# Performance work log

Measured on AMD Instinct MI355X. Metric: run time of the kernel, lower is better.

## Reference

```python
import jax, jax.numpy as jnp
import numpy as np

N_NODES = 50000
DROPOUT_P = 0.5


def _spmm(edge_src, edge_dst, edge_weight, h):
    # out[d] = sum_{e: dst[e]==d} w[e] * h[src[e]]  -- sparse Laplacian aggregation
    msgs = edge_weight[:, None] * h[edge_src]          # [E, F]
    return jax.ops.segment_sum(msgs, edge_dst, num_segments=N_NODES)


def setup_inputs() -> dict:
    key = jax.random.key(0)
    ks = jax.random.split(key, 8)
    E = 1600000
    nfeat, nhid, nclass = 512, 256, 40
    return {
        "x": jax.random.normal(ks[0], (N_NODES, nfeat), dtype=jnp.float32),
        "edge_src": jax.random.randint(ks[1], (E,), 0, N_NODES, dtype=jnp.int32),
        "edge_dst": jax.random.randint(ks[2], (E,), 0, N_NODES, dtype=jnp.int32),
        "edge_weight": jax.random.normal(ks[3], (E,), dtype=jnp.float32) * 0.05,
        "W1": jax.random.normal(ks[4], (nfeat, nhid), dtype=jnp.float32) * 0.05,
        "b1": jax.random.normal(ks[5], (nhid,), dtype=jnp.float32) * 0.05,
        "W2": jax.random.normal(ks[6], (nhid, nclass), dtype=jnp.float32) * 0.05,
        "b2": jax.random.normal(ks[7], (nclass,), dtype=jnp.float32) * 0.05,
    }


def reference(x, edge_src, edge_dst, edge_weight, W1, b1, W2, b2):
    # layer 1: dense GEMM -> sparse aggregate -> bias -> ReLU -> dropout
    h = x @ W1
    h = _spmm(edge_src, edge_dst, edge_weight, h)
    h = jax.nn.relu(h + b1)
    # dropout with a fixed key (deterministic, matches train-mode scaling 1/(1-p))
    keep = jax.random.bernoulli(jax.random.key(42), 1.0 - DROPOUT_P, h.shape)
    h = jnp.where(keep, h / (1.0 - DROPOUT_P), 0.0)
    # layer 2: dense GEMM -> sparse aggregate -> bias
    o = h @ W2
    o = _spmm(edge_src, edge_dst, edge_weight, o)
    return o + b2
```

## Files before the change

### kernel.cpp

```cpp
#include <hip/hip_runtime.h>

typedef short bf16x8 __attribute__((ext_vector_type(8)));
typedef float f32x4 __attribute__((ext_vector_type(4)));

constexpr int N_NODES = 50000;
constexpr int F_IN    = 512;
constexpr int F_HID   = 256;
constexpr int F_OUT   = 40;
constexpr int SCAN_BLOCKS = (N_NODES + 255) / 256;

__device__ __forceinline__ float bf2f(unsigned short u) {
  return __uint_as_float(((unsigned)u) << 16);
}
__device__ __forceinline__ unsigned short f2bf(float f) {
  unsigned x = __float_as_uint(f);
  x += 0x7FFFu + ((x >> 16) & 1u);
  return (unsigned short)(x >> 16);
}

__device__ __forceinline__ bf16x8 cvt8(f32x4 a, f32x4 b) {
  bf16x8 o;
  o[0] = (short)f2bf(a[0]); o[1] = (short)f2bf(a[1]);
  o[2] = (short)f2bf(a[2]); o[3] = (short)f2bf(a[3]);
  o[4] = (short)f2bf(b[0]); o[5] = (short)f2bf(b[1]);
  o[6] = (short)f2bf(b[2]); o[7] = (short)f2bf(b[3]);
  return o;
}

__device__ __forceinline__ unsigned tf_rotl(unsigned x, int d) {
  return (x << d) | (x >> (32 - d));
}
__device__ __forceinline__ unsigned threefry_bits(unsigned i) {
  const unsigned k0 = 0u, k1 = 42u, k2 = 0x1BD11BDAu ^ 0u ^ 42u;
  unsigned x0 = 0u + k0, x1 = i + k1;
#define TF_R(r) { x0 += x1; x1 = tf_rotl(x1, (r)) ^ x0; }
  TF_R(13) TF_R(15) TF_R(26) TF_R(6)   x0 += k1; x1 += k2 + 1u;
  TF_R(17) TF_R(29) TF_R(16) TF_R(24)  x0 += k2; x1 += k0 + 2u;
  TF_R(13) TF_R(15) TF_R(26) TF_R(6)   x0 += k0; x1 += k1 + 3u;
  TF_R(17) TF_R(29) TF_R(16) TF_R(24)  x0 += k1; x1 += k2 + 4u;
  TF_R(13) TF_R(15) TF_R(26) TF_R(6)   x0 += k2; x1 += k0 + 5u;
#undef TF_R
  return x0 ^ x1;
}

__global__ void k_zero(int* __restrict__ p, int n) {
  int i = blockIdx.x * 256 + threadIdx.x;
  if (i < n) p[i] = 0;
}

__global__ void k_hist(const int* __restrict__ dst, int* __restrict__ deg, int E) {
  int e = blockIdx.x * 256 + threadIdx.x;
  if (e < E) atomicAdd(&deg[dst[e]], 1);
}

__global__ __launch_bounds__(256) void k_scan_part(const int* __restrict__ deg,
                                                   int* __restrict__ bsum) {
  __shared__ int red[256];
  int t = threadIdx.x;
  int i = blockIdx.x * 256 + t;
  red[t] = (i < N_NODES) ? deg[i] : 0;
  __syncthreads();
#pragma unroll
  for (int off = 128; off > 0; off >>= 1) {
    if (t < off) red[t] += red[t + off];
    __syncthreads();
  }
  if (t == 0) bsum[blockIdx.x] = red[0];
}

__global__ __launch_bounds__(256) void k_scan_base(int* __restrict__ bsum,
                                                   int* __restrict__ offs) {
  __shared__ int sh[256];
  int t = threadIdx.x;
  int v = (t < SCAN_BLOCKS) ? bsum[t] : 0;
  sh[t] = v;
  __syncthreads();
#pragma unroll
  for (int off = 1; off < 256; off <<= 1) {
    int x = (t >= off) ? sh[t - off] : 0;
    __syncthreads();
    sh[t] += x;
    __syncthreads();
  }
  if (t < SCAN_BLOCKS) bsum[t] = sh[t] - v;
  if (t == 255) offs[N_NODES] = sh[255];
}

__global__ __launch_bounds__(256) void k_scan_final(int* __restrict__ deg,
                                                    const int* __restrict__ bsum,
                                                    int* __restrict__ offs) {
  __shared__ int sh[256];
  int t = threadIdx.x;
  int i = blockIdx.x * 256 + t;
  int v = (i < N_NODES) ? deg[i] : 0;
  sh[t] = v;
  __syncthreads();
#pragma unroll
  for (int off = 1; off < 256; off <<= 1) {
    int x = (t >= off) ? sh[t - off] : 0;
    __syncthreads();
    sh[t] += x;
    __syncthreads();
  }
  if (i < N_NODES) {
    offs[i] = bsum[blockIdx.x] + sh[t] - v;
    deg[i] = 0;
  }
}

__global__ void k_scatter(const int* __restrict__ src, const int* __restrict__ dst,
                          const float* __restrict__ w,
                          const int* __restrict__ offs, int* __restrict__ cursor,
                          unsigned* __restrict__ ep, int E) {
  int e = blockIdx.x * 256 + threadIdx.x;
  if (e < E) {
    int d = dst[e];
    int pos = offs[d] + atomicAdd(&cursor[d], 1);
    if (pos >= 0 && pos < E)
      ep[pos] = ((unsigned)src[e] << 16) | (unsigned)f2bf(w[e]);
  }
}

__global__ void k_wt(const float* __restrict__ W1, unsigned short* __restrict__ wT) {
  int i = blockIdx.x * 256 + threadIdx.x;
  if (i < F_IN * F_HID) {
    int c = i >> 9, k = i & 511;
    wT[i] = f2bf(W1[(size_t)k * F_HID + c]);
  }
}

__global__ __launch_bounds__(256) void k_gemm1m(const float* __restrict__ X,
                                                const unsigned short* __restrict__ wT,
                                                unsigned short* __restrict__ h1h,
                                                int half) {
  int t = threadIdx.x;
  int wave = t >> 6, lane = t & 63, q = lane >> 4, r = lane & 15;
  int r0 = blockIdx.x * 64;
  int arow = r0 + wave * 16 + r;
  if (arow > N_NODES - 1) arow = N_NODES - 1;
  const float* xrow = X + (size_t)arow * F_IN + q * 8;
  const unsigned short* bl = wT + (size_t)half * 128 * F_IN + (size_t)r * F_IN + q * 8;
  f32x4 acc[8];
#pragma unroll
  for (int n = 0; n < 8; ++n) acc[n] = (f32x4){0.f, 0.f, 0.f, 0.f};

#pragma unroll 2
  for (int k0 = 0; k0 < F_IN; k0 += 64) {
    f32x4 a0 = *(const f32x4*)(xrow + k0);
    f32x4 a1 = *(const f32x4*)(xrow + k0 + 4);
    f32x4 a2 = *(const f32x4*)(xrow + k0 + 32);
    f32x4 a3 = *(const f32x4*)(xrow + k0 + 32 + 4);
    bf16x8 A0 = cvt8(a0, a1);
    bf16x8 A1 = cvt8(a2, a3);
#pragma unroll
    for (int n = 0; n < 8; ++n) {
      bf16x8 b0 = *(const bf16x8*)(bl + (size_t)n * 16 * F_IN + k0);
      acc[n] = __builtin_amdgcn_mfma_f32_16x16x32_bf16(A0, b0, acc[n], 0, 0, 0);
    }
#pragma unroll
    for (int n = 0; n < 8; ++n) {
      bf16x8 b1 = *(const bf16x8*)(bl + (size_t)n * 16 * F_IN + k0 + 32);
      acc[n] = __builtin_amdgcn_mfma_f32_16x16x32_bf16(A1, b1, acc[n], 0, 0, 0);
    }
  }
  int mrow = r0 + wave * 16 + q * 4;
#pragma unroll
  for (int n = 0; n < 8; ++n) {
#pragma unroll
    for (int tt = 0; tt < 4; ++tt) {
      int row = mrow + tt;
      if (row < N_NODES) h1h[(size_t)row * 128 + n * 16 + r] = f2bf(acc[n][tt]);
    }
  }
}

__global__ __launch_bounds__(256) void k_agg1h(const ushort2* __restrict__ h1h2,
                                               const int* __restrict__ offs,
                                               const unsigned* __restrict__ ep,
                                               const float* __restrict__ b1,
                                               const float* __restrict__ W2,
                                               float* __restrict__ o1, int half) {
  __shared__ unsigned short w2h[128 * F_OUT];
  __shared__ float hrow[4][128];
  int t = threadIdx.x;
  for (int i = t; i < 128 * F_OUT; i += 256) {
    int k = i / F_OUT, j = i - k * F_OUT;
    w2h[i] = f2bf(W2[(size_t)(half * 128 + k) * F_OUT + j]);
  }
  int wave = t >> 6, lane = t & 63;
  int wid = blockIdx.x * 4 + wave;
  int s0 = offs[wid], s1 = offs[wid + 1];
  float a0 = 0.f, a1 = 0.f;
  int e = s0;
  for (; e + 4 <= s1; e += 4) {
    unsigned p0 = ep[e], p1 = ep[e + 1], p2 = ep[e + 2], p3 = ep[e + 3];
    ushort2 v0 = h1h2[(size_t)(p0 >> 16) * 64 + lane];
    ushort2 v1 = h1h2[(size_t)(p1 >> 16) * 64 + lane];
    ushort2 v2 = h1h2[(size_t)(p2 >> 16) * 64 + lane];
    ushort2 v3 = h1h2[(size_t)(p3 >> 16) * 64 + lane];
    float w0 = bf2f((unsigned short)p0), w1 = bf2f((unsigned short)p1);
    float w2 = bf2f((unsigned short)p2), w3 = bf2f((unsigned short)p3);
    a0 = fmaf(w0, bf2f(v0.x), a0); a1 = fmaf(w0, bf2f(v0.y), a1);
    a0 = fmaf(w1, bf2f(v1.x), a0); a1 = fmaf(w1, bf2f(v1.y), a1);
    a0 = fmaf(w2, bf2f(v2.x), a0); a1 = fmaf(w2, bf2f(v2.y), a1);
    a0 = fmaf(w3, bf2f(v3.x), a0); a1 = fmaf(w3, bf2f(v3.y), a1);
  }
  for (; e < s1; ++e) {
    unsigned pe = ep[e];
    float w = bf2f((unsigned short)pe);
    ushort2 v = h1h2[(size_t)(pe >> 16) * 64 + lane];
    a0 = fmaf(w, bf2f(v.x), a0);
    a1 = fmaf(w, bf2f(v.y), a1);
  }
  int c0 = lane * 2;
  int gc = half * 128 + c0;
  float r0 = fmaxf(a0 + b1[gc + 0], 0.f);
  float r1 = fmaxf(a1 + b1[gc + 1], 0.f);
  unsigned base = (unsigned)wid * 256u + (unsigned)gc;
  r0 = (threefry_bits(base + 0u) >> 31) ? 0.f : r0 * 2.f;
  r1 = (threefry_bits(base + 1u) >> 31) ? 0.f : r1 * 2.f;
  hrow[wave][c0 + 0] = r0;
  hrow[wave][c0 + 1] = r1;
  __syncthreads();
  if (lane < F_OUT) {
    float acc = 0.f;
#pragma unroll 8
    for (int k = 0; k < 128; ++k)
      acc = fmaf(hrow[wave][k], bf2f(w2h[k * F_OUT + lane]), acc);
    o1[(size_t)wid * F_OUT + lane] += acc;
  }
}

__global__ __launch_bounds__(256) void k_agg2(const float* __restrict__ o1,
                                              const int* __restrict__ offs,
                                              const unsigned* __restrict__ ep,
                                              const float* __restrict__ b2,
                                              float* __restrict__ out) {
  int wid  = (blockIdx.x << 2) + (threadIdx.x >> 6);
  int lane = threadIdx.x & 63;
  if (lane >= F_OUT) return;
  int s0 = offs[wid], s1 = offs[wid + 1];
  float acc = 0.f;
  int e = s0;
  for (; e + 4 <= s1; e += 4) {
    unsigned p0 = ep[e], p1 = ep[e + 1], p2 = ep[e + 2], p3 = ep[e + 3];
    float g0 = o1[(size_t)(p0 >> 16) * F_OUT + lane];
    float g1 = o1[(size_t)(p1 >> 16) * F_OUT + lane];
    float g2 = o1[(size_t)(p2 >> 16) * F_OUT + lane];
    float g3 = o1[(size_t)(p3 >> 16) * F_OUT + lane];
    acc = fmaf(bf2f((unsigned short)p0), g0, acc);
    acc = fmaf(bf2f((unsigned short)p1), g1, acc);
    acc = fmaf(bf2f((unsigned short)p2), g2, acc);
    acc = fmaf(bf2f((unsigned short)p3), g3, acc);
  }
  for (; e < s1; ++e) {
    unsigned pe = ep[e];
    acc = fmaf(bf2f((unsigned short)pe), o1[(size_t)(pe >> 16) * F_OUT + lane], acc);
  }
  out[(size_t)wid * F_OUT + lane] = acc + b2[lane];
}

extern "C" void kernel_launch(void* const* d_in, const int* in_sizes, int n_in,
                              void* d_out, int out_size, void* d_ws, size_t ws_size,
                              hipStream_t stream) {
  const float* x    = (const float*)d_in[0];
  const int*   esrc = (const int*)d_in[1];
  const int*   edst = (const int*)d_in[2];
  const float* ew   = (const float*)d_in[3];
  const float* W1   = (const float*)d_in[4];
  const float* b1   = (const float*)d_in[5];
  const float* W2   = (const float*)d_in[6];
  const float* b2   = (const float*)d_in[7];
  const int E = in_sizes[1];

  char* p = (char*)d_ws;
  auto alloc = [&](size_t bytes) { char* r = p; p += (bytes + 255) & ~(size_t)255; return r; };
  unsigned short* h1h  = (unsigned short*)alloc((size_t)N_NODES * 128 * 2);
  float*          o1   = (float*)alloc((size_t)N_NODES * F_OUT * 4);
  unsigned*       ep   = (unsigned*)alloc((size_t)E * 4);
  unsigned short* wT   = (unsigned short*)alloc((size_t)F_IN * F_HID * 2);
  int*            offs = (int*)alloc((size_t)(N_NODES + 1) * 4);
  int*            deg  = (int*)alloc((size_t)N_NODES * 4);
  int*            bsum = (int*)alloc((size_t)SCAN_BLOCKS * 4);

  int eb = (E + 255) / 256;
  k_zero<<<(N_NODES + 255) / 256, 256, 0, stream>>>(deg, N_NODES);
  k_zero<<<(N_NODES * F_OUT + 255) / 256, 256, 0, stream>>>((int*)o1, N_NODES * F_OUT);
  k_wt<<<(F_IN * F_HID + 255) / 256, 256, 0, stream>>>(W1, wT);
  k_hist<<<eb, 256, 0, stream>>>(edst, deg, E);
  k_scan_part<<<SCAN_BLOCKS, 256, 0, stream>>>(deg, bsum);
  k_scan_base<<<1, 256, 0, stream>>>(bsum, offs);
  k_scan_final<<<SCAN_BLOCKS, 256, 0, stream>>>(deg, bsum, offs);
  k_scatter<<<eb, 256, 0, stream>>>(esrc, edst, ew, offs, deg, ep, E);

  int gblocks = (N_NODES + 63) / 64;
  for (int half = 0; half < 2; ++half) {
    k_gemm1m<<<gblocks, 256, 0, stream>>>(x, wT, h1h, half);
    k_agg1h<<<N_NODES / 4, 256, 0, stream>>>((const ushort2*)h1h, offs, ep, b1, W2, o1, half);
  }
  k_agg2<<<N_NODES / 4, 256, 0, stream>>>(o1, offs, ep, b2, (float*)d_out);
}
```

Baseline: 700.8 us.

## Prefetch GEMM B fragments and split edges across half-waves in aggregation

The GEMM kernel fully unrolls the K loop and double-buffers the W1 fragments in registers, loading the next K slice while the current MFMAs run so load latency is hidden. The layer-1 aggregation now has each half-wave handle alternate edges, with each lane gathering 4 bf16 features (8-byte loads) instead of 2. The two halves are combined with a cross-lane shuffle before bias, ReLU and dropout. This aims for wider gathers and more edges in flight, at the cost of more registers and an extra reduction step.

```diff
diff --git a/kernel.cpp b/kernel.cpp
--- a/kernel.cpp
+++ b/kernel.cpp
@@ -144,24 +144,33 @@
 #pragma unroll
   for (int n = 0; n < 8; ++n) acc[n] = (f32x4){0.f, 0.f, 0.f, 0.f};
 
-#pragma unroll 2
+  bf16x8 BA[8], BB[8];
+#pragma unroll
+  for (int n = 0; n < 8; ++n)
+    BA[n] = *(const bf16x8*)(bl + (size_t)n * 16 * F_IN);
+
+#pragma unroll
   for (int k0 = 0; k0 < F_IN; k0 += 64) {
     f32x4 a0 = *(const f32x4*)(xrow + k0);
     f32x4 a1 = *(const f32x4*)(xrow + k0 + 4);
     f32x4 a2 = *(const f32x4*)(xrow + k0 + 32);
-    f32x4 a3 = *(const f32x4*)(xrow + k0 + 32 + 4);
+    f32x4 a3 = *(const f32x4*)(xrow + k0 + 36);
     bf16x8 A0 = cvt8(a0, a1);
     bf16x8 A1 = cvt8(a2, a3);
 #pragma unroll
-    for (int n = 0; n < 8; ++n) {
-      bf16x8 b0 = *(const bf16x8*)(bl + (size_t)n * 16 * F_IN + k0);
-      acc[n] = __builtin_amdgcn_mfma_f32_16x16x32_bf16(A0, b0, acc[n], 0, 0, 0);
+    for (int n = 0; n < 8; ++n)
+      BB[n] = *(const bf16x8*)(bl + (size_t)n * 16 * F_IN + k0 + 32);
+#pragma unroll
+    for (int n = 0; n < 8; ++n)
+      acc[n] = __builtin_amdgcn_mfma_f32_16x16x32_bf16(A0, BA[n], acc[n], 0, 0, 0);
+    if (k0 + 64 < F_IN) {
+#pragma unroll
+      for (int n = 0; n < 8; ++n)
+        BA[n] = *(const bf16x8*)(bl + (size_t)n * 16 * F_IN + k0 + 64);
     }
 #pragma unroll
-    for (int n = 0; n < 8; ++n) {
-      bf16x8 b1 = *(const bf16x8*)(bl + (size_t)n * 16 * F_IN + k0 + 32);
-      acc[n] = __builtin_amdgcn_mfma_f32_16x16x32_bf16(A1, b1, acc[n], 0, 0, 0);
-    }
+    for (int n = 0; n < 8; ++n)
+      acc[n] = __builtin_amdgcn_mfma_f32_16x16x32_bf16(A1, BB[n], acc[n], 0, 0, 0);
   }
   int mrow = r0 + wave * 16 + q * 4;
 #pragma unroll
@@ -174,7 +183,7 @@
   }
 }
 
-__global__ __launch_bounds__(256) void k_agg1h(const ushort2* __restrict__ h1h2,
+__global__ __launch_bounds__(256) void k_agg1h(const unsigned short* __restrict__ h1h,
                                                const int* __restrict__ offs,
                                                const unsigned* __restrict__ ep,
                                                const float* __restrict__ b1,
@@ -188,39 +197,59 @@
     w2h[i] = f2bf(W2[(size_t)(half * 128 + k) * F_OUT + j]);
   }
   int wave = t >> 6, lane = t & 63;
+  int sub = lane >> 5, j = lane & 31;
   int wid = blockIdx.x * 4 + wave;
   int s0 = offs[wid], s1 = offs[wid + 1];
-  float a0 = 0.f, a1 = 0.f;
+  float a0 = 0.f, a1 = 0.f, a2 = 0.f, a3 = 0.f;
+  const unsigned short* hb = h1h + (size_t)j * 4;
   int e = s0;
   for (; e + 4 <= s1; e += 4) {
     unsigned p0 = ep[e], p1 = ep[e + 1], p2 = ep[e + 2], p3 = ep[e + 3];
-    ushort2 v0 = h1h2[(size_t)(p0 >> 16) * 64 + lane];
-    ushort2 v1 = h1h2[(size_t)(p1 >> 16) * 64 + lane];
-    ushort2 v2 = h1h2[(size_t)(p2 >> 16) * 64 + lane];
-    ushort2 v3 = h1h2[(size_t)(p3 >> 16) * 64 + lane];
-    float w0 = bf2f((unsigned short)p0), w1 = bf2f((unsigned short)p1);
-    float w2 = bf2f((unsigned short)p2), w3 = bf2f((unsigned short)p3);
-    a0 = fmaf(w0, bf2f(v0.x), a0); a1 = fmaf(w0, bf2f(v0.y), a1);
-    a0 = fmaf(w1, bf2f(v1.x), a0); a1 = fmaf(w1, bf2f(v1.y), a1);
-    a0 = fmaf(w2, bf2f(v2.x), a0); a1 = fmaf(w2, bf2f(v2.y), a1);
-    a0 = fmaf(w3, bf2f(v3.x), a0); a1 = fmaf(w3, bf2f(v3.y), a1);
-  }
-  for (; e < s1; ++e) {
+    unsigned pa = sub ? p1 : p0;
+    unsigned pb = sub ? p3 : p2;
+    ushort4 va = *(const ushort4*)(hb + (size_t)(pa >> 16) * 128);
+    ushort4 vb = *(const ushort4*)(hb + (size_t)(pb >> 16) * 128);
+    float wa = bf2f((unsigned short)pa);
+    float wb = bf2f((unsigned short)pb);
+    a0 = fmaf(wa, bf2f(va.x), a0); a1 = fmaf(wa, bf2f(va.y), a1);
+    a2 = fmaf(wa, bf2f(va.z), a2); a3 = fmaf(wa, bf2f(va.w), a3);
+    a0 = fmaf(wb, bf2f(vb.x), a0); a1 = fmaf(wb, bf2f(vb.y), a1);
+    a2 = fmaf(wb, bf2f(vb.z), a2); a3 = fmaf(wb, bf2f(vb.w), a3);
+  }
+  if (e + 2 <= s1) {
+    unsigned p0 = ep[e], p1 = ep[e + 1];
+    unsigned pa = sub ? p1 : p0;
+    ushort4 va = *(const ushort4*)(hb + (size_t)(pa >> 16) * 128);
+    float wa = bf2f((unsigned short)pa);
+    a0 = fmaf(wa, bf2f(va.x), a0); a1 = fmaf(wa, bf2f(va.y), a1);
+    a2 = fmaf(wa, bf2f(va.z), a2); a3 = fmaf(wa, bf2f(va.w), a3);
+    e += 2;
+  }
+  if (e < s1) {
     unsigned pe = ep[e];
-    float w = bf2f((unsigned short)pe);
-    ushort2 v = h1h2[(size_t)(pe >> 16) * 64 + lane];
-    a0 = fmaf(w, bf2f(v.x), a0);
-    a1 = fmaf(w, bf2f(v.y), a1);
-  }
-  int c0 = lane * 2;
-  int gc = half * 128 + c0;
-  float r0 = fmaxf(a0 + b1[gc + 0], 0.f);
-  float r1 = fmaxf(a1 + b1[gc + 1], 0.f);
-  unsigned base = (unsigned)wid * 256u + (unsigned)gc;
-  r0 = (threefry_bits(base + 0u) >> 31) ? 0.f : r0 * 2.f;
-  r1 = (threefry_bits(base + 1u) >> 31) ? 0.f : r1 * 2.f;
-  hrow[wave][c0 + 0] = r0;
-  hrow[wave][c0 + 1] = r1;
+    float wa = sub ? 0.f : bf2f((unsigned short)pe);
+    ushort4 va = *(const ushort4*)(hb + (size_t)(pe >> 16) * 128);
+    a0 = fmaf(wa, bf2f(va.x), a0); a1 = fmaf(wa, bf2f(va.y), a1);
+    a2 = fmaf(wa, bf2f(va.z), a2); a3 = fmaf(wa, bf2f(va.w), a3);
+  }
+  a0 += __shfl_xor(a0, 32, 64);
+  a1 += __shfl_xor(a1, 32, 64);
+  a2 += __shfl_xor(a2, 32, 64);
+  a3 += __shfl_xor(a3, 32, 64);
+  if (sub == 0) {
+    float av0 = a0, av1 = a1, av2 = a2, av3 = a3;
+    int c0 = j * 4;
+    int gc = half * 128 + c0;
+    unsigned base = (unsigned)wid * 256u + (unsigned)gc;
+    float r0 = fmaxf(av0 + b1[gc + 0], 0.f);
+    float r1 = fmaxf(av1 + b1[gc + 1], 0.f);
+    float r2 = fmaxf(av2 + b1[gc + 2], 0.f);
+    float r3 = fmaxf(av3 + b1[gc + 3], 0.f);
+    hrow[wave][c0 + 0] = (threefry_bits(base + 0u) >> 31) ? 0.f : r0 * 2.f;
+    hrow[wave][c0 + 1] = (threefry_bits(base + 1u) >> 31) ? 0.f : r1 * 2.f;
+    hrow[wave][c0 + 2] = (threefry_bits(base + 2u) >> 31) ? 0.f : r2 * 2.f;
+    hrow[wave][c0 + 3] = (threefry_bits(base + 3u) >> 31) ? 0.f : r3 * 2.f;
+  }
   __syncthreads();
   if (lane < F_OUT) {
     float acc = 0.f;
@@ -296,7 +325,7 @@
   int gblocks = (N_NODES + 63) / 64;
   for (int half = 0; half < 2; ++half) {
     k_gemm1m<<<gblocks, 256, 0, stream>>>(x, wT, h1h, half);
-    k_agg1h<<<N_NODES / 4, 256, 0, stream>>>((const ushort2*)h1h, offs, ep, b1, W2, o1, half);
+    k_agg1h<<<N_NODES / 4, 256, 0, stream>>>(h1h, offs, ep, b1, W2, o1, half);
   }
   k_agg2<<<N_NODES / 4, 256, 0, stream>>>(o1, offs, ep, b2, (float*)d_out);
 }
```

Result: no change. 713.1 us (+1.8%).

## Compute full hidden layer in one GEMM and single-pass aggregation when workspace allows

Applied to the files above, without the earlier changes.

When the workspace is large enough to hold the full 256-wide bf16 hidden matrix, a single GEMM launch computes both column halves, and one aggregation kernel gathers all 256 features per node with ushort4 loads. Bias, ReLU, dropout and the W2 projection are then applied in that same kernel, which writes o1 directly and drops the o1 zeroing pass. The CSR edge list is therefore walked once instead of twice for layer 1. The GEMM also double-buffers its W1 fragments in registers and gets a launch-bounds occupancy hint, and the old half-split path remains as a fallback when the workspace is too small.

```diff
diff --git a/kernel.cpp b/kernel.cpp
--- a/kernel.cpp
+++ b/kernel.cpp
@@ -129,39 +129,52 @@
   }
 }
 
-__global__ __launch_bounds__(256) void k_gemm1m(const float* __restrict__ X,
-                                                const unsigned short* __restrict__ wT,
-                                                unsigned short* __restrict__ h1h,
-                                                int half) {
+__global__ __launch_bounds__(256, 4) void k_gemm1(const float* __restrict__ X,
+                                                  const unsigned short* __restrict__ wT,
+                                                  unsigned short* __restrict__ out,
+                                                  int ldh, int half) {
   int t = threadIdx.x;
   int wave = t >> 6, lane = t & 63, q = lane >> 4, r = lane & 15;
-  int r0 = blockIdx.x * 64;
+  int halfsel, tile;
+  if (half < 0) { halfsel = blockIdx.x & 1; tile = blockIdx.x >> 1; }
+  else          { halfsel = half;           tile = blockIdx.x; }
+  int r0 = tile * 64;
+  int colbase = (ldh == 256) ? halfsel * 128 : 0;
   int arow = r0 + wave * 16 + r;
   if (arow > N_NODES - 1) arow = N_NODES - 1;
   const float* xrow = X + (size_t)arow * F_IN + q * 8;
-  const unsigned short* bl = wT + (size_t)half * 128 * F_IN + (size_t)r * F_IN + q * 8;
+  const unsigned short* bl = wT + (size_t)halfsel * 128 * F_IN + (size_t)r * F_IN + q * 8;
   f32x4 acc[8];
 #pragma unroll
   for (int n = 0; n < 8; ++n) acc[n] = (f32x4){0.f, 0.f, 0.f, 0.f};
 
-#pragma unroll 2
+  bf16x8 BA[8], BB[8];
+#pragma unroll
+  for (int n = 0; n < 8; ++n)
+    BA[n] = *(const bf16x8*)(bl + (size_t)n * 16 * F_IN);
+
+#pragma unroll
   for (int k0 = 0; k0 < F_IN; k0 += 64) {
     f32x4 a0 = *(const f32x4*)(xrow + k0);
     f32x4 a1 = *(const f32x4*)(xrow + k0 + 4);
     f32x4 a2 = *(const f32x4*)(xrow + k0 + 32);
-    f32x4 a3 = *(const f32x4*)(xrow + k0 + 32 + 4);
+    f32x4 a3 = *(const f32x4*)(xrow + k0 + 36);
     bf16x8 A0 = cvt8(a0, a1);
     bf16x8 A1 = cvt8(a2, a3);
 #pragma unroll
-    for (int n = 0; n < 8; ++n) {
-      bf16x8 b0 = *(const bf16x8*)(bl + (size_t)n * 16 * F_IN + k0);
-      acc[n] = __builtin_amdgcn_mfma_f32_16x16x32_bf16(A0, b0, acc[n], 0, 0, 0);
+    for (int n = 0; n < 8; ++n)
+      BB[n] = *(const bf16x8*)(bl + (size_t)n * 16 * F_IN + k0 + 32);
+#pragma unroll
+    for (int n = 0; n < 8; ++n)
+      acc[n] = __builtin_amdgcn_mfma_f32_16x16x32_bf16(A0, BA[n], acc[n], 0, 0, 0);
+    if (k0 + 64 < F_IN) {
+#pragma unroll
+      for (int n = 0; n < 8; ++n)
+        BA[n] = *(const bf16x8*)(bl + (size_t)n * 16 * F_IN + k0 + 64);
     }
 #pragma unroll
-    for (int n = 0; n < 8; ++n) {
-      bf16x8 b1 = *(const bf16x8*)(bl + (size_t)n * 16 * F_IN + k0 + 32);
-      acc[n] = __builtin_amdgcn_mfma_f32_16x16x32_bf16(A1, b1, acc[n], 0, 0, 0);
-    }
+    for (int n = 0; n < 8; ++n)
+      acc[n] = __builtin_amdgcn_mfma_f32_16x16x32_bf16(A1, BB[n], acc[n], 0, 0, 0);
   }
   int mrow = r0 + wave * 16 + q * 4;
 #pragma unroll
@@ -169,8 +182,71 @@
 #pragma unroll
     for (int tt = 0; tt < 4; ++tt) {
       int row = mrow + tt;
-      if (row < N_NODES) h1h[(size_t)row * 128 + n * 16 + r] = f2bf(acc[n][tt]);
+      if (row < N_NODES)
+        out[(size_t)row * ldh + colbase + n * 16 + r] = f2bf(acc[n][tt]);
     }
+  }
+}
+
+__global__ __launch_bounds__(256) void k_agg1f(const ushort4* __restrict__ h14,
+                                               const int* __restrict__ offs,
+                                               const unsigned* __restrict__ ep,
+                                               const float* __restrict__ b1,
+                                               const float* __restrict__ W2,
+                                               float* __restrict__ o1) {
+  __shared__ unsigned short w2h[F_HID * F_OUT];
+  __shared__ float hrow[4][F_HID];
+  int t = threadIdx.x;
+  for (int i = t; i < F_HID * F_OUT; i += 256)
+    w2h[i] = f2bf(W2[i]);
+  int wave = t >> 6, lane = t & 63;
+  int wid = blockIdx.x * 4 + wave;
+  int s0 = offs[wid], s1 = offs[wid + 1];
+  float a0 = 0.f, a1 = 0.f, a2 = 0.f, a3 = 0.f;
+  int e = s0;
+  for (; e + 4 <= s1; e += 4) {
+    unsigned p0 = ep[e], p1 = ep[e + 1], p2 = ep[e + 2], p3 = ep[e + 3];
+    ushort4 v0 = h14[(size_t)(p0 >> 16) * 64 + lane];
+    ushort4 v1 = h14[(size_t)(p1 >> 16) * 64 + lane];
+    ushort4 v2 = h14[(size_t)(p2 >> 16) * 64 + lane];
+    ushort4 v3 = h14[(size_t)(p3 >> 16) * 64 + lane];
+    float w0 = bf2f((unsigned short)p0), w1 = bf2f((unsigned short)p1);
+    float w2 = bf2f((unsigned short)p2), w3 = bf2f((unsigned short)p3);
+    a0 = fmaf(w0, bf2f(v0.x), a0); a1 = fmaf(w0, bf2f(v0.y), a1);
+    a2 = fmaf(w0, bf2f(v0.z), a2); a3 = fmaf(w0, bf2f(v0.w), a3);
+    a0 = fmaf(w1, bf2f(v1.x), a0); a1 = fmaf(w1, bf2f(v1.y), a1);
+    a2 = fmaf(w1, bf2f(v1.z), a2); a3 = fmaf(w1, bf2f(v1.w), a3);
+    a0 = fmaf(w2, bf2f(v2.x), a0); a1 = fmaf(w2, bf2f(v2.y), a1);
+    a2 = fmaf(w2, bf2f(v2.z), a2); a3 = fmaf(w2, bf2f(v2.w), a3);
+    a0 = fmaf(w3, bf2f(v3.x), a0); a1 = fmaf(w3, bf2f(v3.y), a1);
+    a2 = fmaf(w3, bf2f(v3.z), a2); a3 = fmaf(w3, bf2f(v3.w), a3);
+  }
+  for (; e < s1; ++e) {
+    unsigned pe = ep[e];
+    float w = bf2f((unsigned short)pe);
+    ushort4 v = h14[(size_t)(pe >> 16) * 64 + lane];
+    a0 = fmaf(w, bf2f(v.x), a0);
+    a1 = fmaf(w, bf2f(v.y), a1);
+    a2 = fmaf(w, bf2f(v.z), a2);
+    a3 = fmaf(w, bf2f(v.w), a3);
+  }
+  int c0 = lane * 4;
+  unsigned base = (unsigned)wid * 256u + (unsigned)c0;
+  float r0 = fmaxf(a0 + b1[c0 + 0], 0.f);
+  float r1 = fmaxf(a1 + b1[c0 + 1], 0.f);
+  float r2 = fmaxf(a2 + b1[c0 + 2], 0.f);
+  float r3 = fmaxf(a3 + b1[c0 + 3], 0.f);
+  hrow[wave][c0 + 0] = (threefry_bits(base + 0u) >> 31) ? 0.f : r0 * 2.f;
+  hrow[wave][c0 + 1] = (threefry_bits(base + 1u) >> 31) ? 0.f : r1 * 2.f;
+  hrow[wave][c0 + 2] = (threefry_bits(base + 2u) >> 31) ? 0.f : r2 * 2.f;
+  hrow[wave][c0 + 3] = (threefry_bits(base + 3u) >> 31) ? 0.f : r3 * 2.f;
+  __syncthreads();
+  if (lane < F_OUT) {
+    float acc = 0.f;
+#pragma unroll 8
+    for (int k = 0; k < F_HID; ++k)
+      acc = fmaf(hrow[wave][k], bf2f(w2h[k * F_OUT + lane]), acc);
+    o1[(size_t)wid * F_OUT + lane] = acc;
   }
 }
 
@@ -273,19 +349,30 @@
   const float* b2   = (const float*)d_in[7];
   const int E = in_sizes[1];
 
+  auto rup = [](size_t b) { return (b + 255) & ~(size_t)255; };
+  const size_t sz_h1full = rup((size_t)N_NODES * 256 * 2);
+  const size_t sz_h1half = rup((size_t)N_NODES * 128 * 2);
+  const size_t sz_o1     = rup((size_t)N_NODES * F_OUT * 4);
+  const size_t sz_ep     = rup((size_t)E * 4);
+  const size_t sz_wT     = rup((size_t)F_IN * F_HID * 2);
+  const size_t sz_offs   = rup((size_t)(N_NODES + 1) * 4);
+  const size_t sz_deg    = rup((size_t)N_NODES * 4);
+  const size_t sz_bsum   = rup((size_t)SCAN_BLOCKS * 4);
+  const size_t tail      = sz_o1 + sz_ep + sz_wT + sz_offs + sz_deg + sz_bsum;
+  const bool   fused     = ws_size >= sz_h1full + tail;
+
   char* p = (char*)d_ws;
-  auto alloc = [&](size_t bytes) { char* r = p; p += (bytes + 255) & ~(size_t)255; return r; };
-  unsigned short* h1h  = (unsigned short*)alloc((size_t)N_NODES * 128 * 2);
-  float*          o1   = (float*)alloc((size_t)N_NODES * F_OUT * 4);
-  unsigned*       ep   = (unsigned*)alloc((size_t)E * 4);
-  unsigned short* wT   = (unsigned short*)alloc((size_t)F_IN * F_HID * 2);
-  int*            offs = (int*)alloc((size_t)(N_NODES + 1) * 4);
-  int*            deg  = (int*)alloc((size_t)N_NODES * 4);
-  int*            bsum = (int*)alloc((size_t)SCAN_BLOCKS * 4);
+  auto alloc = [&](size_t bytes) { char* r = p; p += bytes; return r; };
+  unsigned short* h1   = (unsigned short*)alloc(fused ? sz_h1full : sz_h1half);
+  float*          o1   = (float*)alloc(sz_o1);
+  unsigned*       ep   = (unsigned*)alloc(sz_ep);
+  unsigned short* wT   = (unsigned short*)alloc(sz_wT);
+  int*            offs = (int*)alloc(sz_offs);
+  int*            deg  = (int*)alloc(sz_deg);
+  int*            bsum = (int*)alloc(sz_bsum);
 
   int eb = (E + 255) / 256;
   k_zero<<<(N_NODES + 255) / 256, 256, 0, stream>>>(deg, N_NODES);
-  k_zero<<<(N_NODES * F_OUT + 255) / 256, 256, 0, stream>>>((int*)o1, N_NODES * F_OUT);
   k_wt<<<(F_IN * F_HID + 255) / 256, 256, 0, stream>>>(W1, wT);
   k_hist<<<eb, 256, 0, stream>>>(edst, deg, E);
   k_scan_part<<<SCAN_BLOCKS, 256, 0, stream>>>(deg, bsum);
@@ -294,9 +381,15 @@
   k_scatter<<<eb, 256, 0, stream>>>(esrc, edst, ew, offs, deg, ep, E);
 
   int gblocks = (N_NODES + 63) / 64;
-  for (int half = 0; half < 2; ++half) {
-    k_gemm1m<<<gblocks, 256, 0, stream>>>(x, wT, h1h, half);
-    k_agg1h<<<N_NODES / 4, 256, 0, stream>>>((const ushort2*)h1h, offs, ep, b1, W2, o1, half);
+  if (fused) {
+    k_gemm1<<<gblocks * 2, 256, 0, stream>>>(x, wT, h1, 256, -1);
+    k_agg1f<<<N_NODES / 4, 256, 0, stream>>>((const ushort4*)h1, offs, ep, b1, W2, o1);
+  } else {
+    k_zero<<<(N_NODES * F_OUT + 255) / 256, 256, 0, stream>>>((int*)o1, N_NODES * F_OUT);
+    for (int half = 0; half < 2; ++half) {
+      k_gemm1<<<gblocks, 256, 0, stream>>>(x, wT, h1, 128, half);
+      k_agg1h<<<N_NODES / 4, 256, 0, stream>>>((const ushort2*)h1, offs, ep, b1, W2, o1, half);
+    }
   }
   k_agg2<<<N_NODES / 4, 256, 0, stream>>>(o1, offs, ep, b2, (float*)d_out);
 }
```

New measurement: 641.3 us, median of 2. -8.5%, faster.
